# Performance work log

Measured on AMD Instinct MI355X. Metric: run time of the kernel, lower is better.

The kernel has to match this reference:

```python
import jax, jax.numpy as jnp
import numpy as np

BSZ, IN_DIM, HID, OUT_DIM, N_ITERS = 262144, 64, 128, 64, 30


def setup_inputs() -> dict:
    key = jax.random.key(0)
    ks = jax.random.split(key, 6)
    s_h = 1.0 / np.sqrt(HID)
    s_i = 1.0 / np.sqrt(IN_DIM)
    return {
        "x": jax.random.normal(ks[0], (BSZ, IN_DIM), dtype=jnp.float32),
        "Wz": jax.random.uniform(ks[1], (HID, HID), jnp.float32, -s_h, s_h) * 0.9,  # scaled for contraction
        "Ux": jax.random.uniform(ks[2], (HID, IN_DIM), jnp.float32, -s_i, s_i),
        "b": jax.random.uniform(ks[3], (HID,), jnp.float32, -s_h, s_h),
        "Wd": jax.random.uniform(ks[4], (OUT_DIM, HID), jnp.float32, -s_h, s_h),
        "bd": jax.random.uniform(ks[5], (OUT_DIM,), jnp.float32, -s_h, s_h),
        "n_iters": N_ITERS,
    }


def reference(x, Wz, Ux, b, Wd, bd, n_iters):
    # injection term is iteration-invariant: compute once
    inj = x @ Ux.T + b                     # [B, HID]
    z0 = jnp.zeros((x.shape[0], Wz.shape[0]), dtype=x.dtype)

    def step(z, _):
        z = jax.nn.relu(z @ Wz.T + inj)    # f(z, x)
        return z, None

    z_star, _ = jax.lax.scan(step, z0, None, length=n_iters)
    return z_star @ Wd.T + bd              # decoder Linear
```

## Files before the change

### kernel.cpp

```cpp
#include <hip/hip_runtime.h>


typedef __attribute__((ext_vector_type(8))) __bf16 bf16x8;
typedef __attribute__((ext_vector_type(4))) __bf16 bf16x4;
typedef __attribute__((ext_vector_type(4))) float  floatx4;

#define MFMA16(a, b, c) __builtin_amdgcn_mfma_f32_16x16x32_bf16((a), (b), (c), 0, 0, 0)

static constexpr int kBsz = 262144;
static constexpr int kTM  = 64;

__device__ __forceinline__ bf16x8 cvt_bf16x8(float4 a, float4 b) {
  bf16x8 r;
  r[0] = (__bf16)a.x; r[1] = (__bf16)a.y; r[2] = (__bf16)a.z; r[3] = (__bf16)a.w;
  r[4] = (__bf16)b.x; r[5] = (__bf16)b.y; r[6] = (__bf16)b.z; r[7] = (__bf16)b.w;
  return r;
}

__global__ void __launch_bounds__(256) deq_fused(
    const float* __restrict__ x,
    const float* __restrict__ Wz,
    const float* __restrict__ Ux,
    const float* __restrict__ bvec,
    const float* __restrict__ Wd,
    const float* __restrict__ bd,
    const int*  __restrict__ n_iters_p,
    float* __restrict__ out)
{
  __shared__ __align__(16) __bf16 zl[2][kTM][136];

  const int tid  = threadIdx.x;
  const int lane = tid & 63;
  const int wv   = tid >> 6;
  const int wn   = wv & 1;
  const int wm   = wv >> 1;
  const int l15  = lane & 15;
  const int quad = lane >> 4;
  const int row0 = blockIdx.x * kTM;
  const int iters = *n_iters_p;

  bf16x8 awz[4][4];
#pragma unroll
  for (int nt = 0; nt < 4; ++nt) {
    const int n = 64 * wn + 16 * nt + l15;
#pragma unroll
    for (int ks = 0; ks < 4; ++ks) {
      const float4* p = (const float4*)(Wz + n * 128 + 32 * ks + 8 * quad);
      awz[nt][ks] = cvt_bf16x8(p[0], p[1]);
    }
  }

  floatx4 inj[4][2];
#pragma unroll
  for (int nt = 0; nt < 4; ++nt) {
    const float4 bv = *(const float4*)(bvec + 64 * wn + 16 * nt + 4 * quad);
#pragma unroll
    for (int mt = 0; mt < 2; ++mt) {
      floatx4 v = {bv.x, bv.y, bv.z, bv.w};
      inj[nt][mt] = v;
    }
  }
  {
    bf16x8 aux[4][2];
#pragma unroll
    for (int nt = 0; nt < 4; ++nt) {
      const int n = 64 * wn + 16 * nt + l15;
#pragma unroll
      for (int ks = 0; ks < 2; ++ks) {
        const float4* p = (const float4*)(Ux + n * 64 + 32 * ks + 8 * quad);
        aux[nt][ks] = cvt_bf16x8(p[0], p[1]);
      }
    }
#pragma unroll
    for (int mt = 0; mt < 2; ++mt) {
      const int m = row0 + 32 * wm + 16 * mt + l15;
#pragma unroll
      for (int ks = 0; ks < 2; ++ks) {
        const float4* p = (const float4*)(x + m * 64 + 32 * ks + 8 * quad);
        const bf16x8 bx = cvt_bf16x8(p[0], p[1]);
#pragma unroll
        for (int nt = 0; nt < 4; ++nt)
          inj[nt][mt] = MFMA16(aux[nt][ks], bx, inj[nt][mt]);
      }
    }
  }

#pragma unroll
  for (int mt = 0; mt < 2; ++mt) {
    const int ml = 32 * wm + 16 * mt + l15;
#pragma unroll
    for (int nt = 0; nt < 4; ++nt) {
      bf16x4 z4;
#pragma unroll
      for (int i = 0; i < 4; ++i) z4[i] = (__bf16)fmaxf(inj[nt][mt][i], 0.0f);
      *(bf16x4*)&zl[0][ml][64 * wn + 16 * nt + 4 * quad] = z4;
    }
  }

  int pb = 0;
  for (int t = 0; t < iters - 1; ++t) {
    __syncthreads();
    bf16x8 bz[2][4];
#pragma unroll
    for (int mt = 0; mt < 2; ++mt) {
      const int ml = 32 * wm + 16 * mt + l15;
#pragma unroll
      for (int ks = 0; ks < 4; ++ks)
        bz[mt][ks] = *(const bf16x8*)&zl[pb][ml][32 * ks + 8 * quad];
    }
    const int nb = pb ^ 1;
#pragma unroll
    for (int mt = 0; mt < 2; ++mt) {
      const int ml = 32 * wm + 16 * mt + l15;
#pragma unroll
      for (int nt = 0; nt < 4; ++nt) {
        floatx4 acc = inj[nt][mt];
#pragma unroll
        for (int ks = 0; ks < 4; ++ks)
          acc = MFMA16(awz[nt][ks], bz[mt][ks], acc);
        bf16x4 z4;
#pragma unroll
        for (int i = 0; i < 4; ++i) z4[i] = (__bf16)fmaxf(acc[i], 0.0f);
        *(bf16x4*)&zl[nb][ml][64 * wn + 16 * nt + 4 * quad] = z4;
      }
    }
    pb = nb;
  }
  __syncthreads();

  bf16x8 awd[2][4];
#pragma unroll
  for (int ot = 0; ot < 2; ++ot) {
    const int o = 32 * wn + 16 * ot + l15;
#pragma unroll
    for (int ks = 0; ks < 4; ++ks) {
      const float4* p = (const float4*)(Wd + o * 128 + 32 * ks + 8 * quad);
      awd[ot][ks] = cvt_bf16x8(p[0], p[1]);
    }
  }
#pragma unroll
  for (int mt = 0; mt < 2; ++mt) {
    const int ml = 32 * wm + 16 * mt + l15;
    bf16x8 bz[4];
#pragma unroll
    for (int ks = 0; ks < 4; ++ks)
      bz[ks] = *(const bf16x8*)&zl[pb][ml][32 * ks + 8 * quad];
#pragma unroll
    for (int ot = 0; ot < 2; ++ot) {
      const float4 bv = *(const float4*)(bd + 32 * wn + 16 * ot + 4 * quad);
      floatx4 acc = {bv.x, bv.y, bv.z, bv.w};
#pragma unroll
      for (int ks = 0; ks < 4; ++ks)
        acc = MFMA16(awd[ot][ks], bz[ks], acc);
      float4 ov;
      ov.x = acc[0]; ov.y = acc[1]; ov.z = acc[2]; ov.w = acc[3];
      *(float4*)(out + (size_t)(row0 + ml) * 64 + 32 * wn + 16 * ot + 4 * quad) = ov;
    }
  }
}

extern "C" void kernel_launch(void* const* d_in, const int* in_sizes, int n_in,
                              void* d_out, int out_size, void* d_ws, size_t ws_size,
                              hipStream_t stream) {
  const float* x  = (const float*)d_in[0];
  const float* Wz = (const float*)d_in[1];
  const float* Ux = (const float*)d_in[2];
  const float* b  = (const float*)d_in[3];
  const float* Wd = (const float*)d_in[4];
  const float* bd = (const float*)d_in[5];
  const int* n_it = (const int*)d_in[6];
  float* out = (float*)d_out;
  (void)in_sizes; (void)n_in; (void)d_ws; (void)ws_size; (void)out_size;

  dim3 grid(kBsz / kTM);
  deq_fused<<<grid, 256, 0, stream>>>(x, Wz, Ux, b, Wd, bd, n_it, out);
}
```

Measured before the change: 334.8 us.

## Give each wave its own 16-row slice to drop block-wide barriers in DEQ loop

Reorganises the work split so each wave owns 16 batch rows and all 128 hidden units, rather than four waves sharing 64 rows split along hidden. With each wave reading and writing only its own LDS slice, the per-iteration __syncthreads and the double buffer go away, and LDS shrinks to a single buffer per wave. In exchange each wave keeps the full Wz in registers (32 bf16x8 fragments) plus 8 accumulators, which raises register pressure, while launch_bounds(256,2) asks for at least two blocks per CU. Wd fragments are now loaded inline in the decoder instead of being staged in registers first.

```diff
diff --git a/kernel.cpp b/kernel.cpp
--- a/kernel.cpp
+++ b/kernel.cpp
@@ -9,6 +9,7 @@
 
 static constexpr int kBsz = 262144;
 static constexpr int kTM  = 64;
+static constexpr int kLdsStride = 136;
 
 __device__ __forceinline__ bf16x8 cvt_bf16x8(float4 a, float4 b) {
   bf16x8 r;
@@ -17,7 +18,7 @@
   return r;
 }
 
-__global__ void __launch_bounds__(256) deq_fused(
+__global__ void __launch_bounds__(256, 2) deq_fused(
     const float* __restrict__ x,
     const float* __restrict__ Wz,
     const float* __restrict__ Ux,
@@ -27,22 +28,43 @@
     const int*  __restrict__ n_iters_p,
     float* __restrict__ out)
 {
-  __shared__ __align__(16) __bf16 zl[2][kTM][136];
+  __shared__ __align__(16) __bf16 zl[4][16][kLdsStride];
 
   const int tid  = threadIdx.x;
   const int lane = tid & 63;
   const int wv   = tid >> 6;
-  const int wn   = wv & 1;
-  const int wm   = wv >> 1;
   const int l15  = lane & 15;
   const int quad = lane >> 4;
-  const int row0 = blockIdx.x * kTM;
+  const int grow = blockIdx.x * kTM + 16 * wv + l15;
   const int iters = *n_iters_p;
 
-  bf16x8 awz[4][4];
+  __bf16* zrow = &zl[wv][l15][0];
+
+  floatx4 inj[8];
 #pragma unroll
-  for (int nt = 0; nt < 4; ++nt) {
-    const int n = 64 * wn + 16 * nt + l15;
+  for (int nt = 0; nt < 8; ++nt) {
+    const float4 bv = *(const float4*)(bvec + 16 * nt + 4 * quad);
+    floatx4 v = {bv.x, bv.y, bv.z, bv.w};
+    inj[nt] = v;
+  }
+  {
+#pragma unroll
+    for (int ks = 0; ks < 2; ++ks) {
+      const float4* px = (const float4*)(x + (size_t)grow * 64 + 32 * ks + 8 * quad);
+      const bf16x8 bx = cvt_bf16x8(px[0], px[1]);
+#pragma unroll
+      for (int nt = 0; nt < 8; ++nt) {
+        const int n = 16 * nt + l15;
+        const float4* p = (const float4*)(Ux + n * 64 + 32 * ks + 8 * quad);
+        inj[nt] = MFMA16(cvt_bf16x8(p[0], p[1]), bx, inj[nt]);
+      }
+    }
+  }
+
+  bf16x8 awz[8][4];
+#pragma unroll
+  for (int nt = 0; nt < 8; ++nt) {
+    const int n = 16 * nt + l15;
 #pragma unroll
     for (int ks = 0; ks < 4; ++ks) {
       const float4* p = (const float4*)(Wz + n * 128 + 32 * ks + 8 * quad);
@@ -50,111 +72,55 @@
     }
   }
 
-  floatx4 inj[4][2];
 #pragma unroll
-  for (int nt = 0; nt < 4; ++nt) {
-    const float4 bv = *(const float4*)(bvec + 64 * wn + 16 * nt + 4 * quad);
+  for (int nt = 0; nt < 8; ++nt) {
+    bf16x4 z4;
 #pragma unroll
-    for (int mt = 0; mt < 2; ++mt) {
-      floatx4 v = {bv.x, bv.y, bv.z, bv.w};
-      inj[nt][mt] = v;
-    }
+    for (int i = 0; i < 4; ++i) z4[i] = (__bf16)fmaxf(inj[nt][i], 0.0f);
+    *(bf16x4*)&zrow[16 * nt + 4 * quad] = z4;
   }
-  {
-    bf16x8 aux[4][2];
+
+#pragma unroll 1
+  for (int t = 0; t < iters - 1; ++t) {
+    bf16x8 bz[4];
 #pragma unroll
-    for (int nt = 0; nt < 4; ++nt) {
-      const int n = 64 * wn + 16 * nt + l15;
+    for (int ks = 0; ks < 4; ++ks)
+      bz[ks] = *(const bf16x8*)&zrow[32 * ks + 8 * quad];
+    floatx4 acc[8];
 #pragma unroll
-      for (int ks = 0; ks < 2; ++ks) {
-        const float4* p = (const float4*)(Ux + n * 64 + 32 * ks + 8 * quad);
-        aux[nt][ks] = cvt_bf16x8(p[0], p[1]);
-      }
+    for (int nt = 0; nt < 8; ++nt) {
+      acc[nt] = inj[nt];
+#pragma unroll
+      for (int ks = 0; ks < 4; ++ks)
+        acc[nt] = MFMA16(awz[nt][ks], bz[ks], acc[nt]);
     }
 #pragma unroll
-    for (int mt = 0; mt < 2; ++mt) {
-      const int m = row0 + 32 * wm + 16 * mt + l15;
+    for (int nt = 0; nt < 8; ++nt) {
+      bf16x4 z4;
 #pragma unroll
-      for (int ks = 0; ks < 2; ++ks) {
-        const float4* p = (const float4*)(x + m * 64 + 32 * ks + 8 * quad);
-        const bf16x8 bx = cvt_bf16x8(p[0], p[1]);
-#pragma unroll
-        for (int nt = 0; nt < 4; ++nt)
-          inj[nt][mt] = MFMA16(aux[nt][ks], bx, inj[nt][mt]);
-      }
+      for (int i = 0; i < 4; ++i) z4[i] = (__bf16)fmaxf(acc[nt][i], 0.0f);
+      *(bf16x4*)&zrow[16 * nt + 4 * quad] = z4;
     }
   }
 
-#pragma unroll
-  for (int mt = 0; mt < 2; ++mt) {
-    const int ml = 32 * wm + 16 * mt + l15;
-#pragma unroll
-    for (int nt = 0; nt < 4; ++nt) {
-      bf16x4 z4;
-#pragma unroll
-      for (int i = 0; i < 4; ++i) z4[i] = (__bf16)fmaxf(inj[nt][mt][i], 0.0f);
-      *(bf16x4*)&zl[0][ml][64 * wn + 16 * nt + 4 * quad] = z4;
-    }
-  }
-
-  int pb = 0;
-  for (int t = 0; t < iters - 1; ++t) {
-    __syncthreads();
-    bf16x8 bz[2][4];
-#pragma unroll
-    for (int mt = 0; mt < 2; ++mt) {
-      const int ml = 32 * wm + 16 * mt + l15;
-#pragma unroll
-      for (int ks = 0; ks < 4; ++ks)
-        bz[mt][ks] = *(const bf16x8*)&zl[pb][ml][32 * ks + 8 * quad];
-    }
-    const int nb = pb ^ 1;
-#pragma unroll
-    for (int mt = 0; mt < 2; ++mt) {
-      const int ml = 32 * wm + 16 * mt + l15;
-#pragma unroll
-      for (int nt = 0; nt < 4; ++nt) {
-        floatx4 acc = inj[nt][mt];
-#pragma unroll
-        for (int ks = 0; ks < 4; ++ks)
-          acc = MFMA16(awz[nt][ks], bz[mt][ks], acc);
-        bf16x4 z4;
-#pragma unroll
-        for (int i = 0; i < 4; ++i) z4[i] = (__bf16)fmaxf(acc[i], 0.0f);
-        *(bf16x4*)&zl[nb][ml][64 * wn + 16 * nt + 4 * quad] = z4;
-      }
-    }
-    pb = nb;
-  }
-  __syncthreads();
-
-  bf16x8 awd[2][4];
-#pragma unroll
-  for (int ot = 0; ot < 2; ++ot) {
-    const int o = 32 * wn + 16 * ot + l15;
-#pragma unroll
-    for (int ks = 0; ks < 4; ++ks) {
-      const float4* p = (const float4*)(Wd + o * 128 + 32 * ks + 8 * quad);
-      awd[ot][ks] = cvt_bf16x8(p[0], p[1]);
-    }
-  }
-#pragma unroll
-  for (int mt = 0; mt < 2; ++mt) {
-    const int ml = 32 * wm + 16 * mt + l15;
+  {
     bf16x8 bz[4];
 #pragma unroll
     for (int ks = 0; ks < 4; ++ks)
-      bz[ks] = *(const bf16x8*)&zl[pb][ml][32 * ks + 8 * quad];
+      bz[ks] = *(const bf16x8*)&zrow[32 * ks + 8 * quad];
 #pragma unroll
-    for (int ot = 0; ot < 2; ++ot) {
-      const float4 bv = *(const float4*)(bd + 32 * wn + 16 * ot + 4 * quad);
+    for (int ot = 0; ot < 4; ++ot) {
+      const int o = 16 * ot + l15;
+      const float4 bv = *(const float4*)(bd + 16 * ot + 4 * quad);
       floatx4 acc = {bv.x, bv.y, bv.z, bv.w};
 #pragma unroll
-      for (int ks = 0; ks < 4; ++ks)
-        acc = MFMA16(awd[ot][ks], bz[ks], acc);
+      for (int ks = 0; ks < 4; ++ks) {
+        const float4* p = (const float4*)(Wd + o * 128 + 32 * ks + 8 * quad);
+        acc = MFMA16(cvt_bf16x8(p[0], p[1]), bz[ks], acc);
+      }
       float4 ov;
       ov.x = acc[0]; ov.y = acc[1]; ov.z = acc[2]; ov.w = acc[3];
-      *(float4*)(out + (size_t)(row0 + ml) * 64 + 32 * wn + 16 * ot + 4 * quad) = ov;
+      *(float4*)(out + (size_t)grow * 64 + 16 * ot + 4 * quad) = ov;
     }
   }
 }
```

New measurement: 428.3 us. +28.0%, slower.
